# Optimization experiments

Measured on AMD Instinct MI355X. Metric: run time of the kernel, lower is better.

## Reference

```python
import jax, jax.numpy as jnp
import numpy as np

BS, D, S, K = 32, 64, 2048, 1024  # batch, embedding_dim, seq_len, num_embeddings


def setup_inputs() -> dict:
    key = jax.random.key(0)
    k1, k2 = jax.random.split(key)
    x = jax.random.normal(k1, (BS, D, S), dtype=jnp.float32)
    # xavier_uniform on [D, K]
    bound = float(np.sqrt(6.0 / (D + K)))
    embeddings = jax.random.uniform(k2, (D, K), dtype=jnp.float32, minval=-bound, maxval=bound)
    return {"x": x, "embeddings": embeddings}


def reference(x, embeddings):
    bs, d, s = x.shape
    k = embeddings.shape[1]
    # [bs, d, s] -> [bs*s, d]
    flat = x.transpose(0, 2, 1).reshape(-1, d)
    unquantized = flat
    # squared distance ||a||^2 - 2 a.b + ||b||^2 -> [N, K]
    a2 = jnp.sum(flat * flat, axis=1, keepdims=True)
    ab2 = 2.0 * (flat @ embeddings)
    b2 = jnp.sum(embeddings * embeddings, axis=0, keepdims=True)
    distance = a2 - ab2 + b2
    encoding_indices = jnp.argmin(distance, axis=1)  # == (-distance).argmax(1)
    one_hot = jax.nn.one_hot(encoding_indices, k, dtype=jnp.int32)  # F.one_hot -> int
    quantized = jnp.take(embeddings.T, encoding_indices, axis=0)  # [N, d] gather
    quantized = quantized.reshape(bs, s, d).transpose(0, 2, 1)  # [bs, d, s]
    e_latent_loss = jnp.mean(jnp.square(quantized - jax.lax.stop_gradient(x)))
    q_latent_loss = jnp.mean(jnp.square(jax.lax.stop_gradient(quantized) - x))
    loss = q_latent_loss + e_latent_loss
    # straight-through estimator
    quantized_st = x + jax.lax.stop_gradient(quantized - x)
    return (
        quantized_st,
        loss,
        one_hot.reshape(bs, s, k).transpose(0, 2, 1),
        encoding_indices.reshape(bs, s),
        distance.reshape(bs, s, k).transpose(0, 2, 1),
        unquantized,
        embeddings.T,
    )
```

## Files before the change

kernel.cpp:

```cpp
#include <hip/hip_runtime.h>

#define BSZ 32
#define DIM 64
#define SEQ 2048
#define KE  1024
#define KC  128
#define ST  128

#define O0 0ull
#define O1 4194304ull
#define O2 4194305ull
#define O3 71303169ull
#define O4 71368705ull
#define O5 138477569ull
#define O6 142671873ull

struct __attribute__((packed, aligned(4))) F4 { float x, y, z, w; };

__device__ __forceinline__ void lds_barrier() {
    asm volatile("s_waitcnt lgkmcnt(0)" ::: "memory");
    __builtin_amdgcn_s_barrier();
}

__global__ __launch_bounds__(256) void vq_prep(const float* __restrict__ E,
                                               float* __restrict__ out,
                                               float* __restrict__ et_ws,
                                               float* __restrict__ b2_ws) {
    __shared__ float T[64][65];
    const int tid  = threadIdx.x;
    const int lane = tid & 63;
    const int sub  = tid >> 6;
    const int k0   = blockIdx.x * 64;
    for (int dd = 0; dd < 16; ++dd) {
        int d = dd * 4 + sub;
        T[d][lane] = E[(size_t)d * KE + k0 + lane];
    }
    __syncthreads();
    for (int ii = 0; ii < 16; ++ii) {
        int kl = ii * 4 + sub;
        float v = T[lane][kl];
        out[O6 + (size_t)(k0 + kl) * 64 + lane] = v;
        et_ws[(size_t)(k0 + kl) * 64 + lane]    = v;
    }
    if (tid < 64) {
        float s = 0.f;
        #pragma unroll
        for (int d = 0; d < 64; ++d) {
            float v = T[d][tid];
            s = fmaf(v, v, s);
        }
        b2_ws[k0 + tid] = s;
    }
    if (blockIdx.x == 0 && tid == 0) out[O1] = 0.f;
}

__global__ __launch_bounds__(512, 4) void vq_main(const float* __restrict__ x,
                                                  const float* __restrict__ E,
                                                  const float* __restrict__ et,
                                                  const float* __restrict__ b2,
                                                  float* __restrict__ out) {
    __shared__ __align__(16) float xt[64 * ST];
    __shared__ __align__(16) union UU {
        float e[64 * KC];
        struct { float D[16][ST]; int Kk[16][ST]; } red;
    } u;
    __shared__ __align__(16) float a2s[ST];

    const int tid = threadIdx.x;
    const int tx  = tid & 31;
    const int ky  = tid >> 5;
    const int b   = blockIdx.x >> 4;
    const int s0  = (blockIdx.x & 15) << 7;
    const int sq  = tx << 2;

    float4 er[4];
    #pragma unroll
    for (int i = 0; i < 4; ++i) {
        int f = (i << 9) + tid, d = f >> 5, j = f & 31;
        er[i] = *(const float4*)(E + (size_t)d * KE + (j << 2));
    }
    {
        const float* xb = x + ((size_t)b << 17) + s0;
        #pragma unroll
        for (int i = 0; i < 4; ++i) {
            int f = (i << 9) + tid, d = f >> 5, j = f & 31;
            *(float4*)&xt[d * ST + (j << 2)] =
                *(const float4*)(xb + ((size_t)d << 11) + (j << 2));
        }
    }
    __syncthreads();
    if (tid < ST) {
        float sacc = 0.f;
        #pragma unroll
        for (int d = 0; d < 64; ++d) { float v = xt[d * ST + tid]; sacc = fmaf(v, v, sacc); }
        a2s[tid] = sacc;
    }

    float bD[4]; int bK[4];
    #pragma unroll
    for (int j = 0; j < 4; ++j) { bD[j] = 3.4e38f; bK[j] = 0; }

    float* outD = out + O4 + ((size_t)b << 21) + s0;
    float* outH = out + O2 + ((size_t)b << 21) + s0;

    #pragma unroll 1
    for (int c = 0; c < KE / KC; ++c) {
        const int kc = c << 7;
        lds_barrier();
        #pragma unroll
        for (int i = 0; i < 4; ++i) {
            int f = (i << 9) + tid, d = f >> 5, j = f & 31;
            *(float4*)&u.e[d * KC + (j << 2)] = er[i];
        }
        lds_barrier();
        if (c < KE / KC - 1) {
            #pragma unroll
            for (int i = 0; i < 4; ++i) {
                int f = (i << 9) + tid, d = f >> 5, j = f & 31;
                er[i] = *(const float4*)(E + (size_t)d * KE + (kc + KC) + (j << 2));
            }
        }

        float acc[8][4];
        #pragma unroll
        for (int jk = 0; jk < 8; ++jk)
            #pragma unroll
            for (int js = 0; js < 4; ++js) acc[jk][js] = 0.f;

        #pragma unroll 2
        for (int d = 0; d < 64; ++d) {
            float4 xa = *(const float4*)&xt[d * ST + sq];
            float4 ea = *(const float4*)&u.e[d * KC + (ky << 3)];
            float4 eb = *(const float4*)&u.e[d * KC + (ky << 3) + 4];
            float xs[4] = {xa.x, xa.y, xa.z, xa.w};
            float es[8] = {ea.x, ea.y, ea.z, ea.w, eb.x, eb.y, eb.z, eb.w};
            #pragma unroll
            for (int jk = 0; jk < 8; ++jk)
                #pragma unroll
                for (int js = 0; js < 4; ++js)
                    acc[jk][js] = fmaf(es[jk], xs[js], acc[jk][js]);
        }

        float4 b2a = *(const float4*)(b2 + kc + (ky << 3));
        float4 b2b = *(const float4*)(b2 + kc + (ky << 3) + 4);
        float b2v[8] = {b2a.x, b2a.y, b2a.z, b2a.w, b2b.x, b2b.y, b2b.z, b2b.w};
        float4 av = *(const float4*)&a2s[sq];
        float a2v[4] = {av.x, av.y, av.z, av.w};
        #pragma unroll
        for (int jk = 0; jk < 8; ++jk) {
            const int k = kc + (ky << 3) + jk;
            float dv[4];
            #pragma unroll
            for (int js = 0; js < 4; ++js) {
                dv[js] = fmaf(-2.f, acc[jk][js], a2v[js] + b2v[jk]);
                if (dv[js] < bD[js]) { bD[js] = dv[js]; bK[js] = k; }
            }
            float* pD = outD + ((size_t)k << 11);
            float* pH = outH + ((size_t)k << 11);
            *(F4*)(pD + sq) = F4{dv[0], dv[1], dv[2], dv[3]};
            *(F4*)(pH + sq) = F4{0.f, 0.f, 0.f, 0.f};
        }
    }

    lds_barrier();
    #pragma unroll
    for (int js = 0; js < 4; ++js) {
        u.red.D[ky][sq + js]  = bD[js];
        u.red.Kk[ky][sq + js] = bK[js];
    }
    __syncthreads();

    if (tid < ST) {
        float bDr = u.red.D[0][tid];
        int   bKr = u.red.Kk[0][tid];
        #pragma unroll
        for (int w = 1; w < 16; ++w) {
            float dw = u.red.D[w][tid];
            int   kw = u.red.Kk[w][tid];
            if (dw < bDr || (dw == bDr && kw < bKr)) { bDr = dw; bKr = kw; }
        }
        out[O3 + (size_t)b * SEQ + s0 + tid] = (float)bKr;
        out[O2 + ((size_t)b << 21) + ((size_t)bKr << 11) + s0 + tid] = 1.f;

        const float* q = et + ((size_t)bKr << 6);
        float* outQ = out + ((size_t)b << 17) + s0 + tid;
        float lsum = 0.f;
        #pragma unroll
        for (int i = 0; i < 16; ++i) {
            float4 q4 = ((const float4*)q)[i];
            float qs[4] = {q4.x, q4.y, q4.z, q4.w};
            #pragma unroll
            for (int j = 0; j < 4; ++j) {
                int d = i * 4 + j;
                outQ[(size_t)d << 11] = qs[j];
                float df = qs[j] - xt[d * ST + tid];
                lsum = fmaf(df, df, lsum);
            }
        }
        #pragma unroll
        for (int m = 32; m >= 1; m >>= 1) lsum += __shfl_xor(lsum, m, 64);
        if ((tid & 63) == 0) atomicAdd(out + O1, lsum * (2.f / 4194304.f));
    }

    {
        const int lane = tid & 63, sub = tid >> 6;
        float* op = out + O5 + (((size_t)b << 11) + s0) * 64;
        #pragma unroll
        for (int ii = 0; ii < 16; ++ii) {
            int sl = ii * 8 + sub;
            op[(size_t)sl * 64 + lane] = xt[lane * ST + sl];
        }
    }
}

extern "C" void kernel_launch(void* const* d_in, const int* in_sizes, int n_in,
                              void* d_out, int out_size, void* d_ws, size_t ws_size,
                              hipStream_t stream) {
    const float* x = (const float*)d_in[0];
    const float* E = (const float*)d_in[1];
    float* out   = (float*)d_out;
    float* et_ws = (float*)d_ws;
    float* b2_ws = et_ws + 65536;
    vq_prep<<<16, 256, 0, stream>>>(E, out, et_ws, b2_ws);
    vq_main<<<512, 512, 0, stream>>>(x, E, et_ws, b2_ws, out);
}
```

Measured before the change: 238.8 us.

## Split VQ into distance kernel with larger tiles and separate one-hot/quantize post kernel

Enlarges the distance tile to 256 sequence positions by 256 codes per block, with 16x8 per-thread register accumulators. Codebook and x tiles are loaded with direct global-to-LDS loads, and the next codebook chunk is prefetched asynchronously after the compute. The one-hot zero writes, the quantized gather, the loss and the unquantized transpose move into a new post kernel that runs once per column, which makes one-hot writing a single pass with no scattered 1.0 overwrite. The risks are that the grid shrinks to 256 blocks with a heavier register footprint, which lowers occupancy, and that the extra launch re-reads x.

```diff
diff --git a/kernel.cpp b/kernel.cpp
--- a/kernel.cpp
+++ b/kernel.cpp
@@ -1,11 +1,10 @@
 #include <hip/hip_runtime.h>
+#include <stdint.h>
 
 #define BSZ 32
 #define DIM 64
 #define SEQ 2048
 #define KE  1024
-#define KC  128
-#define ST  128
 
 #define O0 0ull
 #define O1 4194304ull
@@ -20,6 +19,12 @@
 __device__ __forceinline__ void lds_barrier() {
     asm volatile("s_waitcnt lgkmcnt(0)" ::: "memory");
     __builtin_amdgcn_s_barrier();
+}
+
+__device__ __forceinline__ void gl_lds16(const float* g, float* l) {
+    __builtin_amdgcn_global_load_lds(
+        (const __attribute__((address_space(1))) uint32_t*)g,
+        (__attribute__((address_space(3))) uint32_t*)l, 16, 0, 0);
 }
 
 __global__ __launch_bounds__(256) void vq_prep(const float* __restrict__ E,
@@ -54,163 +59,176 @@
     if (blockIdx.x == 0 && tid == 0) out[O1] = 0.f;
 }
 
-__global__ __launch_bounds__(512, 4) void vq_main(const float* __restrict__ x,
+__global__ __launch_bounds__(512, 2) void vq_dist(const float* __restrict__ x,
                                                   const float* __restrict__ E,
-                                                  const float* __restrict__ et,
                                                   const float* __restrict__ b2,
                                                   float* __restrict__ out) {
-    __shared__ __align__(16) float xt[64 * ST];
-    __shared__ __align__(16) union UU {
-        float e[64 * KC];
-        struct { float D[16][ST]; int Kk[16][ST]; } red;
-    } u;
-    __shared__ __align__(16) float a2s[ST];
+    __shared__ __align__(16) float xt[64 * 256];
+    __shared__ __align__(16) float ebuf[64 * 256];
+    __shared__ __align__(16) float a2s[256];
 
     const int tid = threadIdx.x;
     const int tx  = tid & 31;
     const int ky  = tid >> 5;
-    const int b   = blockIdx.x >> 4;
-    const int s0  = (blockIdx.x & 15) << 7;
+    const int b   = blockIdx.x >> 3;
+    const int s0  = (blockIdx.x & 7) << 8;
     const int sq  = tx << 2;
-
-    float4 er[4];
-    #pragma unroll
-    for (int i = 0; i < 4; ++i) {
-        int f = (i << 9) + tid, d = f >> 5, j = f & 31;
-        er[i] = *(const float4*)(E + (size_t)d * KE + (j << 2));
-    }
-    {
-        const float* xb = x + ((size_t)b << 17) + s0;
-        #pragma unroll
-        for (int i = 0; i < 4; ++i) {
-            int f = (i << 9) + tid, d = f >> 5, j = f & 31;
-            *(float4*)&xt[d * ST + (j << 2)] =
-                *(const float4*)(xb + ((size_t)d << 11) + (j << 2));
-        }
-    }
-    __syncthreads();
-    if (tid < ST) {
+    const int kq  = ky << 4;
+
+    const float* xb = x + ((size_t)b << 17) + s0;
+    #pragma unroll
+    for (int i = 0; i < 8; ++i) {
+        int f = (i << 9) + tid;
+        int d = f >> 6, c4 = (f & 63) << 2;
+        gl_lds16(xb + ((size_t)d << 11) + c4, &xt[(d << 8) + c4]);
+    }
+    #pragma unroll
+    for (int i = 0; i < 8; ++i) {
+        int f = (i << 9) + tid;
+        int d = f >> 6, c4 = (f & 63) << 2;
+        gl_lds16(E + (size_t)d * KE + c4, &ebuf[(d << 8) + c4]);
+    }
+    asm volatile("s_waitcnt vmcnt(0)" ::: "memory");
+    __builtin_amdgcn_s_barrier();
+
+    if (tid < 256) {
         float sacc = 0.f;
         #pragma unroll
-        for (int d = 0; d < 64; ++d) { float v = xt[d * ST + tid]; sacc = fmaf(v, v, sacc); }
+        for (int d = 0; d < 64; ++d) { float v = xt[(d << 8) + tid]; sacc = fmaf(v, v, sacc); }
         a2s[tid] = sacc;
     }
-
-    float bD[4]; int bK[4];
-    #pragma unroll
-    for (int j = 0; j < 4; ++j) { bD[j] = 3.4e38f; bK[j] = 0; }
-
+    lds_barrier();
+    float4 av0 = *(const float4*)&a2s[sq];
+    float4 av1 = *(const float4*)&a2s[128 + sq];
+    const float a2v[8] = {av0.x, av0.y, av0.z, av0.w, av1.x, av1.y, av1.z, av1.w};
+
+    float bD[8]; int bK[8];
+    #pragma unroll
+    for (int j = 0; j < 8; ++j) { bD[j] = 3.4e38f; bK[j] = 0; }
     float* outD = out + O4 + ((size_t)b << 21) + s0;
-    float* outH = out + O2 + ((size_t)b << 21) + s0;
 
     #pragma unroll 1
-    for (int c = 0; c < KE / KC; ++c) {
-        const int kc = c << 7;
-        lds_barrier();
-        #pragma unroll
-        for (int i = 0; i < 4; ++i) {
-            int f = (i << 9) + tid, d = f >> 5, j = f & 31;
-            *(float4*)&u.e[d * KC + (j << 2)] = er[i];
-        }
-        lds_barrier();
-        if (c < KE / KC - 1) {
-            #pragma unroll
-            for (int i = 0; i < 4; ++i) {
-                int f = (i << 9) + tid, d = f >> 5, j = f & 31;
-                er[i] = *(const float4*)(E + (size_t)d * KE + (kc + KC) + (j << 2));
-            }
-        }
-
-        float acc[8][4];
-        #pragma unroll
-        for (int jk = 0; jk < 8; ++jk)
-            #pragma unroll
-            for (int js = 0; js < 4; ++js) acc[jk][js] = 0.f;
+    for (int c = 0; c < 4; ++c) {
+        const int kc = c << 8;
+        if (c > 0) {
+            asm volatile("s_waitcnt vmcnt(32)" ::: "memory");
+            __builtin_amdgcn_s_barrier();
+        }
+        float4 bb0 = *(const float4*)(b2 + kc + kq);
+        float4 bb1 = *(const float4*)(b2 + kc + kq + 4);
+        float4 bb2 = *(const float4*)(b2 + kc + kq + 8);
+        float4 bb3 = *(const float4*)(b2 + kc + kq + 12);
+
+        float acc[16][8];
+        #pragma unroll
+        for (int jk = 0; jk < 16; ++jk)
+            #pragma unroll
+            for (int js = 0; js < 8; ++js) acc[jk][js] = 0.f;
 
         #pragma unroll 2
         for (int d = 0; d < 64; ++d) {
-            float4 xa = *(const float4*)&xt[d * ST + sq];
-            float4 ea = *(const float4*)&u.e[d * KC + (ky << 3)];
-            float4 eb = *(const float4*)&u.e[d * KC + (ky << 3) + 4];
-            float xs[4] = {xa.x, xa.y, xa.z, xa.w};
-            float es[8] = {ea.x, ea.y, ea.z, ea.w, eb.x, eb.y, eb.z, eb.w};
-            #pragma unroll
-            for (int jk = 0; jk < 8; ++jk)
+            const float* xp = &xt[d << 8];
+            const float* ep = &ebuf[(d << 8) + kq];
+            float4 xa = *(const float4*)(xp + sq);
+            float4 xc = *(const float4*)(xp + 128 + sq);
+            float4 e0 = *(const float4*)(ep);
+            float4 e1 = *(const float4*)(ep + 4);
+            float4 e2 = *(const float4*)(ep + 8);
+            float4 e3 = *(const float4*)(ep + 12);
+            float xs[8]  = {xa.x, xa.y, xa.z, xa.w, xc.x, xc.y, xc.z, xc.w};
+            float es[16] = {e0.x, e0.y, e0.z, e0.w, e1.x, e1.y, e1.z, e1.w,
+                            e2.x, e2.y, e2.z, e2.w, e3.x, e3.y, e3.z, e3.w};
+            #pragma unroll
+            for (int jk = 0; jk < 16; ++jk)
                 #pragma unroll
-                for (int js = 0; js < 4; ++js)
+                for (int js = 0; js < 8; ++js)
                     acc[jk][js] = fmaf(es[jk], xs[js], acc[jk][js]);
         }
-
-        float4 b2a = *(const float4*)(b2 + kc + (ky << 3));
-        float4 b2b = *(const float4*)(b2 + kc + (ky << 3) + 4);
-        float b2v[8] = {b2a.x, b2a.y, b2a.z, b2a.w, b2b.x, b2b.y, b2b.z, b2b.w};
-        float4 av = *(const float4*)&a2s[sq];
-        float a2v[4] = {av.x, av.y, av.z, av.w};
-        #pragma unroll
-        for (int jk = 0; jk < 8; ++jk) {
-            const int k = kc + (ky << 3) + jk;
-            float dv[4];
-            #pragma unroll
-            for (int js = 0; js < 4; ++js) {
+        lds_barrier();
+        if (c < 3) {
+            #pragma unroll
+            for (int i = 0; i < 8; ++i) {
+                int f = (i << 9) + tid;
+                int d = f >> 6, c4 = (f & 63) << 2;
+                gl_lds16(E + (size_t)d * KE + (kc + 256) + c4, &ebuf[(d << 8) + c4]);
+            }
+        }
+        const float b2v[16] = {bb0.x, bb0.y, bb0.z, bb0.w, bb1.x, bb1.y, bb1.z, bb1.w,
+                               bb2.x, bb2.y, bb2.z, bb2.w, bb3.x, bb3.y, bb3.z, bb3.w};
+        #pragma unroll
+        for (int jk = 0; jk < 16; ++jk) {
+            const int k = kc + kq + jk;
+            float dv[8];
+            #pragma unroll
+            for (int js = 0; js < 8; ++js) {
                 dv[js] = fmaf(-2.f, acc[jk][js], a2v[js] + b2v[jk]);
                 if (dv[js] < bD[js]) { bD[js] = dv[js]; bK[js] = k; }
             }
             float* pD = outD + ((size_t)k << 11);
-            float* pH = outH + ((size_t)k << 11);
-            *(F4*)(pD + sq) = F4{dv[0], dv[1], dv[2], dv[3]};
-            *(F4*)(pH + sq) = F4{0.f, 0.f, 0.f, 0.f};
+            *(F4*)(pD + sq)       = F4{dv[0], dv[1], dv[2], dv[3]};
+            *(F4*)(pD + 128 + sq) = F4{dv[4], dv[5], dv[6], dv[7]};
         }
     }
 
     lds_barrier();
-    #pragma unroll
-    for (int js = 0; js < 4; ++js) {
-        u.red.D[ky][sq + js]  = bD[js];
-        u.red.Kk[ky][sq + js] = bK[js];
+    float* rD = ebuf;
+    int*   rK = (int*)(ebuf + 4096);
+    #pragma unroll
+    for (int js = 0; js < 8; ++js) {
+        int sl = sq + (js & 3) + ((js >> 2) << 7);
+        rD[(ky << 8) + sl] = bD[js];
+        rK[(ky << 8) + sl] = bK[js];
     }
     __syncthreads();
-
-    if (tid < ST) {
-        float bDr = u.red.D[0][tid];
-        int   bKr = u.red.Kk[0][tid];
+    if (tid < 256) {
+        float bDr = rD[tid]; int bKr = rK[tid];
         #pragma unroll
         for (int w = 1; w < 16; ++w) {
-            float dw = u.red.D[w][tid];
-            int   kw = u.red.Kk[w][tid];
+            float dw = rD[(w << 8) + tid];
+            int   kw = rK[(w << 8) + tid];
             if (dw < bDr || (dw == bDr && kw < bKr)) { bDr = dw; bKr = kw; }
         }
         out[O3 + (size_t)b * SEQ + s0 + tid] = (float)bKr;
-        out[O2 + ((size_t)b << 21) + ((size_t)bKr << 11) + s0 + tid] = 1.f;
-
-        const float* q = et + ((size_t)bKr << 6);
-        float* outQ = out + ((size_t)b << 17) + s0 + tid;
-        float lsum = 0.f;
-        #pragma unroll
-        for (int i = 0; i < 16; ++i) {
-            float4 q4 = ((const float4*)q)[i];
-            float qs[4] = {q4.x, q4.y, q4.z, q4.w};
-            #pragma unroll
-            for (int j = 0; j < 4; ++j) {
-                int d = i * 4 + j;
-                outQ[(size_t)d << 11] = qs[j];
-                float df = qs[j] - xt[d * ST + tid];
-                lsum = fmaf(df, df, lsum);
-            }
-        }
-        #pragma unroll
-        for (int m = 32; m >= 1; m >>= 1) lsum += __shfl_xor(lsum, m, 64);
-        if ((tid & 63) == 0) atomicAdd(out + O1, lsum * (2.f / 4194304.f));
-    }
-
-    {
-        const int lane = tid & 63, sub = tid >> 6;
-        float* op = out + O5 + (((size_t)b << 11) + s0) * 64;
-        #pragma unroll
-        for (int ii = 0; ii < 16; ++ii) {
-            int sl = ii * 8 + sub;
-            op[(size_t)sl * 64 + lane] = xt[lane * ST + sl];
-        }
-    }
+    }
+}
+
+__global__ __launch_bounds__(256) void vq_post(const float* __restrict__ x,
+                                               const float* __restrict__ et,
+                                               float* __restrict__ out) {
+    const int tid = threadIdx.x;
+    const int col = (blockIdx.x << 8) + tid;
+    const int b   = col >> 11;
+    const int s   = col & 2047;
+    const int myk = (int)out[O3 + col];
+
+    float* pH = out + O2 + ((size_t)b << 21) + s;
+    #pragma unroll 8
+    for (int k = 0; k < KE; ++k)
+        pH[(size_t)k << 11] = (k == myk) ? 1.f : 0.f;
+
+    const float* q  = et + ((size_t)myk << 6);
+    const float* xp = x + ((size_t)b << 17) + s;
+    float* oq = out + ((size_t)b << 17) + s;
+    float* ou = out + O5 + (size_t)col * 64;
+    float lsum = 0.f;
+    #pragma unroll
+    for (int i = 0; i < 16; ++i) {
+        float4 q4 = ((const float4*)q)[i];
+        float qs[4] = {q4.x, q4.y, q4.z, q4.w};
+        float xv[4];
+        #pragma unroll
+        for (int j = 0; j < 4; ++j) {
+            int d = (i << 2) + j;
+            xv[j] = xp[(size_t)d << 11];
+            oq[(size_t)d << 11] = qs[j];
+            float df = qs[j] - xv[j];
+            lsum = fmaf(df, df, lsum);
+        }
+        *(F4*)(ou + (i << 2)) = F4{xv[0], xv[1], xv[2], xv[3]};
+    }
+    #pragma unroll
+    for (int m = 32; m >= 1; m >>= 1) lsum += __shfl_xor(lsum, m, 64);
+    if ((tid & 63) == 0) atomicAdd(out + O1, lsum * (2.f / 4194304.f));
 }
 
 extern "C" void kernel_launch(void* const* d_in, const int* in_sizes, int n_in,
@@ -222,5 +240,6 @@
     float* et_ws = (float*)d_ws;
     float* b2_ws = et_ws + 65536;
     vq_prep<<<16, 256, 0, stream>>>(E, out, et_ws, b2_ws);
-    vq_main<<<512, 512, 0, stream>>>(x, E, et_ws, b2_ws, out);
-}
+    vq_dist<<<256, 512, 0, stream>>>(x, E, b2_ws, out);
+    vq_post<<<256, 256, 0, stream>>>(x, et_ws, out);
+}
```

Measured after the change: 268.2 us. 12.3% more time.
